# Kernel tuning notes

Measured on AMD Instinct MI355X. Metric: run time of the kernel, lower is better.

## Reference

```python
import jax, jax.numpy as jnp
import numpy as np

N_HEAD = 16
N_STATE = 1024
D_HEAD = N_STATE // N_HEAD
B, T = 4, 2048


def setup_inputs() -> dict:
    key = jax.random.key(0)
    ks = jax.random.split(key, 9)
    x = jax.random.normal(ks[0], (B, T, N_STATE), dtype=jnp.float32)
    # causal additive mask, (T, T)
    neg = jnp.float32(-1e9)
    mask = jnp.where(jnp.tril(jnp.ones((T, T), dtype=bool)), 0.0, neg).astype(jnp.float32)
    s = 0.02  # keep activations in a sane range (module uses torch.randn init)
    Wq = jax.random.normal(ks[1], (N_STATE, N_STATE), dtype=jnp.float32) * s
    bq = jax.random.normal(ks[2], (N_STATE,), dtype=jnp.float32) * s
    Wk = jax.random.normal(ks[3], (N_STATE, N_STATE), dtype=jnp.float32) * s
    Wv = jax.random.normal(ks[4], (N_STATE, N_STATE), dtype=jnp.float32) * s
    bv = jax.random.normal(ks[5], (N_STATE,), dtype=jnp.float32) * s
    Wo = jax.random.normal(ks[6], (N_STATE, N_STATE), dtype=jnp.float32) * s
    bo = jax.random.normal(ks[7], (N_STATE,), dtype=jnp.float32) * s
    return {"x": x, "mask": mask, "Wq": Wq, "bq": bq, "Wk": Wk,
            "Wv": Wv, "bv": bv, "Wo": Wo, "bo": bo}


def reference(x, mask, Wq, bq, Wk, Wv, bv, Wo, bo):
    n, t, _ = x.shape
    scale = D_HEAD ** -0.25
    # projections: Linear stores weight as (out, in), applies x @ W.T
    q = x @ Wq.T + bq
    k = x @ Wk.T          # key has no bias
    v = x @ Wv.T + bv
    # (N, H, T, d)
    q = q.reshape(n, t, N_HEAD, D_HEAD).transpose(0, 2, 1, 3) * scale
    k = k.reshape(n, t, N_HEAD, D_HEAD).transpose(0, 2, 1, 3) * scale
    v = v.reshape(n, t, N_HEAD, D_HEAD).transpose(0, 2, 1, 3)
    qk = jnp.einsum('bhqd,bhkd->bhqk', q, k)
    qk = qk + mask[:t, :t]
    attn = jax.nn.softmax(qk, axis=-1)
    qkv = jnp.einsum('bhqk,bhkd->bhqd', attn, v)
    qkv = qkv.transpose(0, 2, 1, 3).reshape(n, t, N_STATE)
    return qkv @ Wo.T + bo
```

## Files before the change

kernel.cpp:

```cpp
#include <hip/hip_runtime.h>
#include <stdint.h>

#define DEVI __device__ __forceinline__

typedef float        f32x4   __attribute__((ext_vector_type(4)));
typedef float        f32x16  __attribute__((ext_vector_type(16)));
typedef __bf16       bf16x8  __attribute__((ext_vector_type(8)));
typedef unsigned short u16x8 __attribute__((ext_vector_type(8)));
typedef uint32_t     u32x2   __attribute__((ext_vector_type(2)));
typedef uint32_t     u32x4   __attribute__((ext_vector_type(4)));

static constexpr int TSEQ   = 2048;
static constexpr int NSTATE = 1024;
static constexpr int NHEAD  = 16;
static constexpr int DHEAD  = 64;
static constexpr int BATCH  = 4;
static constexpr int MROWS  = BATCH * TSEQ;
static constexpr float QSCALE = 0.125f * 1.44269504088896340736f;
static constexpr float DEFER_THR = 8.0f * 1.44269504088896340736f;

DEVI unsigned short f2bf(float f) {
  union { float f; uint32_t u; } v; v.f = f;
  return (unsigned short)((v.u + 0x7fffu + ((v.u >> 16) & 1u)) >> 16);
}

DEVI uint32_t cvt_pk_bf16(float lo, float hi) {
  uint32_t r;
  asm("v_cvt_pk_bf16_f32 %0, %1, %2" : "=v"(r) : "v"(lo), "v"(hi));
  return r;
}

DEVI f32x4 mfma16(u16x8 a, u16x8 b, f32x4 c) {
  return __builtin_amdgcn_mfma_f32_16x16x32_bf16(
      __builtin_bit_cast(bf16x8, a), __builtin_bit_cast(bf16x8, b), c, 0, 0, 0);
}
DEVI f32x16 mfma32(u16x8 a, u16x8 b, f32x16 c) {
  return __builtin_amdgcn_mfma_f32_32x32x16_bf16(
      __builtin_bit_cast(bf16x8, a), __builtin_bit_cast(bf16x8, b), c, 0, 0, 0);
}

DEVI void gload_lds16(const void* g, void* l) {
  __builtin_amdgcn_global_load_lds(
      (const __attribute__((address_space(1))) void*)g,
      (__attribute__((address_space(3))) void*)l, 16, 0, 0);
}

__global__ void cvt_kernel(const float* __restrict__ in,
                           unsigned short* __restrict__ out, int n4) {
  int i = blockIdx.x * blockDim.x + threadIdx.x;
  const int stride = gridDim.x * blockDim.x;
  for (; i < n4; i += stride) {
    const float4 f = ((const float4*)in)[i];
    ushort4 o;
    o.x = f2bf(f.x); o.y = f2bf(f.y); o.z = f2bf(f.z); o.w = f2bf(f.w);
    ((ushort4*)out)[i] = o;
  }
}

__global__ void cvt4_kernel(const float* __restrict__ w0, const float* __restrict__ w1,
                            const float* __restrict__ w2, const float* __restrict__ w3,
                            unsigned short* __restrict__ o0, unsigned short* __restrict__ o1,
                            unsigned short* __restrict__ o2, unsigned short* __restrict__ o3) {
  const int per = NSTATE * NSTATE / 4;
  int i = blockIdx.x * blockDim.x + threadIdx.x;
  const int stride = gridDim.x * blockDim.x;
  for (; i < 4 * per; i += stride) {
    const int wi = i / per, j = i - wi * per;
    const float* src = (wi == 0) ? w0 : (wi == 1) ? w1 : (wi == 2) ? w2 : w3;
    unsigned short* dst = (wi == 0) ? o0 : (wi == 1) ? o1 : (wi == 2) ? o2 : o3;
    const float4 f = ((const float4*)src)[j];
    ushort4 o;
    o.x = f2bf(f.x); o.y = f2bf(f.y); o.z = f2bf(f.z); o.w = f2bf(f.w);
    ((ushort4*)dst)[j] = o;
  }
}

__global__ __launch_bounds__(256)
void gemm_qkv(const unsigned short* __restrict__ A,
              const unsigned short* __restrict__ Wqkv,
              const float* __restrict__ bq, const float* __restrict__ bv,
              unsigned short* __restrict__ Oqkv)
{
  __shared__ __align__(16) unsigned short As[128 * 32];
  __shared__ __align__(16) unsigned short Bs[128 * 32];
  const int t  = threadIdx.x;
  const int l  = t & 63, w = t >> 6;
  const int fr = l & 15, fq = l >> 4;
  const int wi = blockIdx.x >> 3;
  const int n0 = (blockIdx.x & 7) * 128;
  const int m0 = blockIdx.y * 128;
  const int wm = (w & 1) * 64, wn = (w >> 1) * 64;
  const unsigned short* Bw = Wqkv + (size_t)wi * (1u << 20);
  unsigned short* Cq = Oqkv + (size_t)wi * (8u << 20);

  f32x4 acc[4][4] = {};

  const int sr = t >> 2;
  const int sc = (t & 3) * 8;
  const unsigned short* ag = A  + (size_t)(m0 + sr) * NSTATE + sc;
  const unsigned short* bg = Bw + (size_t)(n0 + sr) * NSTATE + sc;
  unsigned short* lA0 = As + t * 8;
  unsigned short* lA1 = As + 2048 + t * 8;
  unsigned short* lB0 = Bs + t * 8;
  unsigned short* lB1 = Bs + 2048 + t * 8;

  for (int kt = 0; kt < NSTATE / 32; ++kt) {
    const int ko = kt * 32;
    gload_lds16(ag + ko,               lA0);
    gload_lds16(ag + 64 * NSTATE + ko, lA1);
    gload_lds16(bg + ko,               lB0);
    gload_lds16(bg + 64 * NSTATE + ko, lB1);
    __syncthreads();

    u16x8 a[4], b[4];
    #pragma unroll
    for (int i = 0; i < 4; ++i)
      a[i] = *(const u16x8*)(As + (wm + i * 16 + fr) * 32 + fq * 8);
    #pragma unroll
    for (int j = 0; j < 4; ++j)
      b[j] = *(const u16x8*)(Bs + (wn + j * 16 + fr) * 32 + fq * 8);
    #pragma unroll
    for (int i = 0; i < 4; ++i)
      #pragma unroll
      for (int j = 0; j < 4; ++j)
        acc[i][j] = mfma16(a[i], b[j], acc[i][j]);
    __syncthreads();
  }

  const int h = (n0 + wn) >> 6;
  #pragma unroll
  for (int j = 0; j < 4; ++j) {
    const int d = j * 16 + fr;
    const float bj = (wi == 1) ? 0.0f
                   : ((wi == 0) ? bq[n0 + wn + d] : bv[n0 + wn + d]);
    #pragma unroll
    for (int i = 0; i < 4; ++i) {
      #pragma unroll
      for (int r = 0; r < 4; ++r) {
        const int row = m0 + wm + i * 16 + fq * 4 + r;
        const int bb = row >> 11, tt = row & (TSEQ - 1);
        float v = acc[i][j][r] + bj;
        if (wi == 0) v *= QSCALE;
        Cq[(((size_t)(bb * NHEAD + h)) * TSEQ + tt) * DHEAD + d] = f2bf(v);
      }
    }
  }
}

__global__ __launch_bounds__(256)
void gemm_out(const unsigned short* __restrict__ A,
              const unsigned short* __restrict__ Bw,
              const float* __restrict__ bias,
              float* __restrict__ Co)
{
  __shared__ __align__(16) unsigned short As[128 * 32];
  __shared__ __align__(16) unsigned short Bs[128 * 32];
  const int t  = threadIdx.x;
  const int l  = t & 63, w = t >> 6;
  const int fr = l & 15, fq = l >> 4;
  const int m0 = blockIdx.y * 128, n0 = blockIdx.x * 128;
  const int wm = (w & 1) * 64, wn = (w >> 1) * 64;

  f32x4 acc[4][4] = {};

  const int sr = t >> 2;
  const int sc = (t & 3) * 8;
  const unsigned short* ag = A  + (size_t)(m0 + sr) * NSTATE + sc;
  const unsigned short* bg = Bw + (size_t)(n0 + sr) * NSTATE + sc;
  unsigned short* lA0 = As + t * 8;
  unsigned short* lA1 = As + 2048 + t * 8;
  unsigned short* lB0 = Bs + t * 8;
  unsigned short* lB1 = Bs + 2048 + t * 8;

  for (int kt = 0; kt < NSTATE / 32; ++kt) {
    const int ko = kt * 32;
    gload_lds16(ag + ko,               lA0);
    gload_lds16(ag + 64 * NSTATE + ko, lA1);
    gload_lds16(bg + ko,               lB0);
    gload_lds16(bg + 64 * NSTATE + ko, lB1);
    __syncthreads();

    u16x8 a[4], b[4];
    #pragma unroll
    for (int i = 0; i < 4; ++i)
      a[i] = *(const u16x8*)(As + (wm + i * 16 + fr) * 32 + fq * 8);
    #pragma unroll
    for (int j = 0; j < 4; ++j)
      b[j] = *(const u16x8*)(Bs + (wn + j * 16 + fr) * 32 + fq * 8);
    #pragma unroll
    for (int i = 0; i < 4; ++i)
      #pragma unroll
      for (int j = 0; j < 4; ++j)
        acc[i][j] = mfma16(a[i], b[j], acc[i][j]);
    __syncthreads();
  }

  #pragma unroll
  for (int j = 0; j < 4; ++j) {
    const int col = n0 + wn + j * 16 + fr;
    const float bj = bias[col];
    #pragma unroll
    for (int i = 0; i < 4; ++i) {
      const int row0 = m0 + wm + i * 16 + fq * 4;
      #pragma unroll
      for (int r = 0; r < 4; ++r)
        Co[(size_t)(row0 + r) * NSTATE + col] = acc[i][j][r] + bj;
    }
  }
}

__global__ __launch_bounds__(256)
void flash_attn(const unsigned short* __restrict__ Qg,
                const unsigned short* __restrict__ Kg,
                const unsigned short* __restrict__ Vg,
                unsigned short* __restrict__ O)
{
  const int bh = blockIdx.x;
  const int qb = 15 - (int)blockIdx.y;
  const int b  = bh >> 4, h = bh & 15;
  const int t  = threadIdx.x, lane = t & 63, w = t >> 6;
  const int lq = lane & 31, hi = lane >> 5;
  const size_t hoff = (size_t)bh * TSEQ * DHEAD;
  const unsigned short* Qp = Qg + hoff;
  const unsigned short* Kp = Kg + hoff;
  const unsigned short* Vp = Vg + hoff;

  __shared__ __align__(16) unsigned short Kb[2][64 * 64];
  __shared__ __align__(16) unsigned short Vb[2][64 * 64];

  const int qw   = qb * 128 + w * 32;
  const int qrow = qw + lq;

  u16x8 qf[4];
  #pragma unroll
  for (int c = 0; c < 4; ++c)
    qf[c] = *(const u16x8*)(Qp + (size_t)qrow * DHEAD + c * 16 + hi * 8);

  f32x16 oacc[2] = {};
  float m_r = -1e30f, l_r = 0.0f;

  const int skr = t >> 2, skg = t & 3;
  const int svk2 = (t & 31) * 2;
  const int svd  = (t >> 5) * 8;

  const int nt = (qb + 1) * 2;

  {
    const u16x8 kr0 = *(const u16x8*)(Kp + (size_t)skr * DHEAD + skg * 16);
    const u16x8 kr1 = *(const u16x8*)(Kp + (size_t)skr * DHEAD + skg * 16 + 8);
    const u16x8 va  = *(const u16x8*)(Vp + (size_t)svk2 * DHEAD + svd);
    const u16x8 vb  = *(const u16x8*)(Vp + (size_t)(svk2 + 1) * DHEAD + svd);
    *(u16x8*)(&Kb[0][skr * 64 + (((skg * 2)     ^ (skr & 7)) << 3)]) = kr0;
    *(u16x8*)(&Kb[0][skr * 64 + (((skg * 2 + 1) ^ (skr & 7)) << 3)]) = kr1;
    #pragma unroll
    for (int i = 0; i < 8; ++i)
      *(uint32_t*)(&Vb[0][(svd + i) * 64 + (svk2 ^ (i << 3))]) =
          (uint32_t)va[i] | ((uint32_t)vb[i] << 16);
  }
  __syncthreads();

  for (int kt = 0; kt < nt; ++kt) {
    const int k0 = kt * 64, cur = kt & 1;
    const bool pre = (kt + 1 < nt);
    u16x8 krn0, krn1, van, vbn;
    if (pre) {
      const int k0n = k0 + 64;
      krn0 = *(const u16x8*)(Kp + (size_t)(k0n + skr) * DHEAD + skg * 16);
      krn1 = *(const u16x8*)(Kp + (size_t)(k0n + skr) * DHEAD + skg * 16 + 8);
      van  = *(const u16x8*)(Vp + (size_t)(k0n + svk2) * DHEAD + svd);
      vbn  = *(const u16x8*)(Vp + (size_t)(k0n + svk2 + 1) * DHEAD + svd);
    }

    if (k0 < qw + 32) {
      f32x16 s[2];
      __builtin_amdgcn_s_setprio(1);
      #pragma unroll
      for (int t32 = 0; t32 < 2; ++t32) {
        if (k0 + t32 * 32 < qw + 32) {
          f32x16 z = {};
          #pragma unroll
          for (int c = 0; c < 4; ++c) {
            const u16x8 kf = *(const u16x8*)(
                &Kb[cur][(t32 * 32 + lq) * 64 + (((2 * c + hi) ^ (lane & 7)) << 3)]);
            z = mfma32(kf, qf[c], z);
          }
          s[t32] = z;
        } else {
          #pragma unroll
          for (int r = 0; r < 16; ++r) s[t32][r] = -1e30f;
        }
      }
      __builtin_amdgcn_s_setprio(0);
      if (k0 + 63 > qw) {
        #pragma unroll
        for (int t32 = 0; t32 < 2; ++t32)
          #pragma unroll
          for (int r = 0; r < 16; ++r) {
            const int kk = k0 + t32 * 32 + (r & 3) + 8 * (r >> 2) + 4 * hi;
            if (kk > qrow) s[t32][r] = -1e30f;
          }
      }

      float mx = fmaxf(s[0][14], s[0][15]);
      #pragma unroll
      for (int r = 0; r < 14; r += 2) mx = fmaxf(fmaxf(mx, s[0][r]), s[0][r + 1]);
      #pragma unroll
      for (int r = 0; r < 16; r += 2) mx = fmaxf(fmaxf(mx, s[1][r]), s[1][r + 1]);
      mx = fmaxf(mx, __shfl_xor(mx, 32));

      if (__any(mx > m_r + DEFER_THR)) {
        const float mnew = fmaxf(m_r, mx);
        const float corr = exp2f(m_r - mnew);
        #pragma unroll
        for (int ds = 0; ds < 2; ++ds)
          #pragma unroll
          for (int r = 0; r < 16; ++r) oacc[ds][r] *= corr;
        l_r *= corr;
        m_r = mnew;
      }

      float ps = 0.0f;
      uint32_t pk[2][8];
      #pragma unroll
      for (int t32 = 0; t32 < 2; ++t32)
        #pragma unroll
        for (int m2 = 0; m2 < 8; ++m2) {
          const float pa = exp2f(s[t32][2 * m2]     - m_r);
          const float pb = exp2f(s[t32][2 * m2 + 1] - m_r);
          ps += pa + pb;
          pk[t32][m2] = cvt_pk_bf16(pa, pb);
        }
      ps += __shfl_xor(ps, 32);
      l_r += ps;

      uint32_t pf[2][2][4];
      #pragma unroll
      for (int t32 = 0; t32 < 2; ++t32)
        #pragma unroll
        for (int hf = 0; hf < 2; ++hf) {
          const u32x2 r02 = __builtin_amdgcn_permlane32_swap(
              pk[t32][hf * 4 + 0], pk[t32][hf * 4 + 2], false, false);
          const u32x2 r13 = __builtin_amdgcn_permlane32_swap(
              pk[t32][hf * 4 + 1], pk[t32][hf * 4 + 3], false, false);
          pf[t32][hf][0] = r02.x; pf[t32][hf][2] = r02.y;
          pf[t32][hf][1] = r13.x; pf[t32][hf][3] = r13.y;
        }

      __builtin_amdgcn_s_setprio(1);
      #pragma unroll
      for (int c = 0; c < 4; ++c) {
        if (k0 + 16 * c < qw + 32) {
          const u32x4 pw = {pf[c >> 1][c & 1][0], pf[c >> 1][c & 1][1],
                            pf[c >> 1][c & 1][2], pf[c >> 1][c & 1][3]};
          const u16x8 pv = __builtin_bit_cast(u16x8, pw);
          #pragma unroll
          for (int ds = 0; ds < 2; ++ds) {
            const u16x8 vf = *(const u16x8*)(
                &Vb[cur][(ds * 32 + lq) * 64 + (((2 * c + hi) ^ (lq & 7)) << 3)]);
            oacc[ds] = mfma32(vf, pv, oacc[ds]);
          }
        }
      }
      __builtin_amdgcn_s_setprio(0);
    }

    if (pre) {
      *(u16x8*)(&Kb[cur ^ 1][skr * 64 + (((skg * 2)     ^ (skr & 7)) << 3)]) = krn0;
      *(u16x8*)(&Kb[cur ^ 1][skr * 64 + (((skg * 2 + 1) ^ (skr & 7)) << 3)]) = krn1;
      #pragma unroll
      for (int i = 0; i < 8; ++i)
        *(uint32_t*)(&Vb[cur ^ 1][(svd + i) * 64 + (svk2 ^ (i << 3))]) =
            (uint32_t)van[i] | ((uint32_t)vbn[i] << 16);
    }
    __syncthreads();
  }

  const float inv = 1.0f / l_r;
  const size_t base = ((size_t)(b * TSEQ + qrow)) * NSTATE + h * DHEAD;
  #pragma unroll
  for (int ds = 0; ds < 2; ++ds)
    #pragma unroll
    for (int m2 = 0; m2 < 8; ++m2) {
      const int d = ds * 32 + 2 * (m2 & 1) + 8 * (m2 >> 1) + 4 * hi;
      *(uint32_t*)(O + base + d) =
          cvt_pk_bf16(oacc[ds][2 * m2] * inv, oacc[ds][2 * m2 + 1] * inv);
    }
}

extern "C" void kernel_launch(void* const* d_in, const int* in_sizes, int n_in,
                              void* d_out, int out_size, void* d_ws, size_t ws_size,
                              hipStream_t stream)
{
  (void)in_sizes; (void)n_in; (void)out_size; (void)ws_size;
  const float* x  = (const float*)d_in[0];
  const float* Wq = (const float*)d_in[2];
  const float* bq = (const float*)d_in[3];
  const float* Wk = (const float*)d_in[4];
  const float* Wv = (const float*)d_in[5];
  const float* bv = (const float*)d_in[6];
  const float* Wo = (const float*)d_in[7];
  const float* bo = (const float*)d_in[8];

  char* ws = (char*)d_ws;
  unsigned short* xb  = (unsigned short*)(ws);
  unsigned short* wqb = (unsigned short*)(ws + (16u << 20));
  unsigned short* wkb = wqb + (1u << 20);
  unsigned short* wvb = wkb + (1u << 20);
  unsigned short* wob = wvb + (1u << 20);
  unsigned short* qb_ = (unsigned short*)(ws + (24u << 20));
  unsigned short* kb_ = (unsigned short*)(ws + (40u << 20));
  unsigned short* vb_ = (unsigned short*)(ws + (56u << 20));

  cvt_kernel<<<2048, 256, 0, stream>>>(x,  xb,  MROWS * NSTATE / 4);
  cvt4_kernel<<<2048, 256, 0, stream>>>(Wq, Wk, Wv, Wo, wqb, wkb, wvb, wob);

  gemm_qkv<<<dim3(24, MROWS / 128), 256, 0, stream>>>(xb, wqb, bq, bv, qb_);

  flash_attn<<<dim3(BATCH * NHEAD, 16), 256, 0, stream>>>(qb_, kb_, vb_, xb);

  gemm_out<<<dim3(NSTATE / 128, MROWS / 128), 256, 0, stream>>>(xb, wob, bo, (float*)d_out);
}
```

Before: 199.3 us.

## Double-buffer GEMM LDS tiles, MFMA row sums and reordered causal tiles in attention

Both projection GEMMs now use two LDS buffers. The next K-slice is prefetched with global-to-LDS loads while MFMAs run on the current one, removing one barrier per iteration. The attention kernel computes the softmax row sum with an extra MFMA against a ones matrix instead of VALU adds plus a cross-lane shuffle. It also packs V into LDS with byte-permute instructions and interleaves query-block order across the grid to balance causal work. The cost is doubled LDS use in the GEMMs, which may lower occupancy, and extra MFMA issue in attention.

Measured after the change: 219.8 us. 1.1x slower.

```diff
diff --git a/kernel.cpp b/kernel.cpp
--- a/kernel.cpp
+++ b/kernel.cpp
@@ -81,8 +81,8 @@
               const float* __restrict__ bq, const float* __restrict__ bv,
               unsigned short* __restrict__ Oqkv)
 {
-  __shared__ __align__(16) unsigned short As[128 * 32];
-  __shared__ __align__(16) unsigned short Bs[128 * 32];
+  __shared__ __align__(16) unsigned short As[2][128 * 32];
+  __shared__ __align__(16) unsigned short Bs[2][128 * 32];
   const int t  = threadIdx.x;
   const int l  = t & 63, w = t >> 6;
   const int fr = l & 15, fq = l >> 4;
@@ -99,26 +99,30 @@
   const int sc = (t & 3) * 8;
   const unsigned short* ag = A  + (size_t)(m0 + sr) * NSTATE + sc;
   const unsigned short* bg = Bw + (size_t)(n0 + sr) * NSTATE + sc;
-  unsigned short* lA0 = As + t * 8;
-  unsigned short* lA1 = As + 2048 + t * 8;
-  unsigned short* lB0 = Bs + t * 8;
-  unsigned short* lB1 = Bs + 2048 + t * 8;
-
+
+  #define STAGE_G(buf, ko)                                              \
+    do {                                                                \
+      gload_lds16(ag + (ko),               &As[buf][t * 8]);            \
+      gload_lds16(ag + 64 * NSTATE + (ko), &As[buf][2048 + t * 8]);     \
+      gload_lds16(bg + (ko),               &Bs[buf][t * 8]);            \
+      gload_lds16(bg + 64 * NSTATE + (ko), &Bs[buf][2048 + t * 8]);     \
+    } while (0)
+
+  STAGE_G(0, 0);
+  __syncthreads();
+
+  #pragma unroll 2
   for (int kt = 0; kt < NSTATE / 32; ++kt) {
-    const int ko = kt * 32;
-    gload_lds16(ag + ko,               lA0);
-    gload_lds16(ag + 64 * NSTATE + ko, lA1);
-    gload_lds16(bg + ko,               lB0);
-    gload_lds16(bg + 64 * NSTATE + ko, lB1);
-    __syncthreads();
+    const int cur = kt & 1;
+    if (kt + 1 < NSTATE / 32) STAGE_G(cur ^ 1, (kt + 1) * 32);
 
     u16x8 a[4], b[4];
     #pragma unroll
     for (int i = 0; i < 4; ++i)
-      a[i] = *(const u16x8*)(As + (wm + i * 16 + fr) * 32 + fq * 8);
+      a[i] = *(const u16x8*)(&As[cur][(wm + i * 16 + fr) * 32 + fq * 8]);
     #pragma unroll
     for (int j = 0; j < 4; ++j)
-      b[j] = *(const u16x8*)(Bs + (wn + j * 16 + fr) * 32 + fq * 8);
+      b[j] = *(const u16x8*)(&Bs[cur][(wn + j * 16 + fr) * 32 + fq * 8]);
     #pragma unroll
     for (int i = 0; i < 4; ++i)
       #pragma unroll
@@ -153,8 +157,8 @@
               const float* __restrict__ bias,
               float* __restrict__ Co)
 {
-  __shared__ __align__(16) unsigned short As[128 * 32];
-  __shared__ __align__(16) unsigned short Bs[128 * 32];
+  __shared__ __align__(16) unsigned short As[2][128 * 32];
+  __shared__ __align__(16) unsigned short Bs[2][128 * 32];
   const int t  = threadIdx.x;
   const int l  = t & 63, w = t >> 6;
   const int fr = l & 15, fq = l >> 4;
@@ -167,26 +171,22 @@
   const int sc = (t & 3) * 8;
   const unsigned short* ag = A  + (size_t)(m0 + sr) * NSTATE + sc;
   const unsigned short* bg = Bw + (size_t)(n0 + sr) * NSTATE + sc;
-  unsigned short* lA0 = As + t * 8;
-  unsigned short* lA1 = As + 2048 + t * 8;
-  unsigned short* lB0 = Bs + t * 8;
-  unsigned short* lB1 = Bs + 2048 + t * 8;
-
+
+  STAGE_G(0, 0);
+  __syncthreads();
+
+  #pragma unroll 2
   for (int kt = 0; kt < NSTATE / 32; ++kt) {
-    const int ko = kt * 32;
-    gload_lds16(ag + ko,               lA0);
-    gload_lds16(ag + 64 * NSTATE + ko, lA1);
-    gload_lds16(bg + ko,               lB0);
-    gload_lds16(bg + 64 * NSTATE + ko, lB1);
-    __syncthreads();
+    const int cur = kt & 1;
+    if (kt + 1 < NSTATE / 32) STAGE_G(cur ^ 1, (kt + 1) * 32);
 
     u16x8 a[4], b[4];
     #pragma unroll
     for (int i = 0; i < 4; ++i)
-      a[i] = *(const u16x8*)(As + (wm + i * 16 + fr) * 32 + fq * 8);
+      a[i] = *(const u16x8*)(&As[cur][(wm + i * 16 + fr) * 32 + fq * 8]);
     #pragma unroll
     for (int j = 0; j < 4; ++j)
-      b[j] = *(const u16x8*)(Bs + (wn + j * 16 + fr) * 32 + fq * 8);
+      b[j] = *(const u16x8*)(&Bs[cur][(wn + j * 16 + fr) * 32 + fq * 8]);
     #pragma unroll
     for (int i = 0; i < 4; ++i)
       #pragma unroll
@@ -216,7 +216,8 @@
                 unsigned short* __restrict__ O)
 {
   const int bh = blockIdx.x;
-  const int qb = 15 - (int)blockIdx.y;
+  const int yy = blockIdx.y, ai = yy & 3, ii = yy >> 2;
+  const int qb = (ii == 0) ? 15 - ai : (ii == 1) ? ai : (ii == 2) ? 8 + ai : 7 - ai;
   const int b  = bh >> 4, h = bh & 15;
   const int t  = threadIdx.x, lane = t & 63, w = t >> 6;
   const int lq = lane & 31, hi = lane >> 5;
@@ -236,14 +237,31 @@
   for (int c = 0; c < 4; ++c)
     qf[c] = *(const u16x8*)(Qp + (size_t)qrow * DHEAD + c * 16 + hi * 8);
 
+  const u16x8 ones8 = {0x3F80, 0x3F80, 0x3F80, 0x3F80,
+                       0x3F80, 0x3F80, 0x3F80, 0x3F80};
+
   f32x16 oacc[2] = {};
-  float m_r = -1e30f, l_r = 0.0f;
+  f32x16 lacc = {};
+  float m_r = -1e30f;
 
   const int skr = t >> 2, skg = t & 3;
   const int svk2 = (t & 31) * 2;
   const int svd  = (t >> 5) * 8;
 
   const int nt = (qb + 1) * 2;
+
+  #define STAGE_V(buf, va, vb)                                              \
+    do {                                                                    \
+      const u32x4 vau = __builtin_bit_cast(u32x4, va);                      \
+      const u32x4 vbu = __builtin_bit_cast(u32x4, vb);                      \
+      _Pragma("unroll")                                                     \
+      for (int j = 0; j < 4; ++j) {                                         \
+        const uint32_t pe = __builtin_amdgcn_perm(vbu[j], vau[j], 0x05040100); \
+        const uint32_t po = __builtin_amdgcn_perm(vbu[j], vau[j], 0x07060302); \
+        *(uint32_t*)(&Vb[buf][(svd + 2 * j) * 64 + (svk2 ^ ((2 * j) << 3))]) = pe; \
+        *(uint32_t*)(&Vb[buf][(svd + 2 * j + 1) * 64 + (svk2 ^ ((2 * j + 1) << 3))]) = po; \
+      }                                                                     \
+    } while (0)
 
   {
     const u16x8 kr0 = *(const u16x8*)(Kp + (size_t)skr * DHEAD + skg * 16);
@@ -252,10 +270,7 @@
     const u16x8 vb  = *(const u16x8*)(Vp + (size_t)(svk2 + 1) * DHEAD + svd);
     *(u16x8*)(&Kb[0][skr * 64 + (((skg * 2)     ^ (skr & 7)) << 3)]) = kr0;
     *(u16x8*)(&Kb[0][skr * 64 + (((skg * 2 + 1) ^ (skr & 7)) << 3)]) = kr1;
-    #pragma unroll
-    for (int i = 0; i < 8; ++i)
-      *(uint32_t*)(&Vb[0][(svd + i) * 64 + (svk2 ^ (i << 3))]) =
-          (uint32_t)va[i] | ((uint32_t)vb[i] << 16);
+    STAGE_V(0, va, vb);
   }
   __syncthreads();
 
@@ -315,11 +330,10 @@
         for (int ds = 0; ds < 2; ++ds)
           #pragma unroll
           for (int r = 0; r < 16; ++r) oacc[ds][r] *= corr;
-        l_r *= corr;
+        lacc[0] *= corr;
         m_r = mnew;
       }
 
-      float ps = 0.0f;
       uint32_t pk[2][8];
       #pragma unroll
       for (int t32 = 0; t32 < 2; ++t32)
@@ -327,11 +341,8 @@
         for (int m2 = 0; m2 < 8; ++m2) {
           const float pa = exp2f(s[t32][2 * m2]     - m_r);
           const float pb = exp2f(s[t32][2 * m2 + 1] - m_r);
-          ps += pa + pb;
           pk[t32][m2] = cvt_pk_bf16(pa, pb);
         }
-      ps += __shfl_xor(ps, 32);
-      l_r += ps;
 
       uint32_t pf[2][2][4];
       #pragma unroll
@@ -359,6 +370,7 @@
                 &Vb[cur][(ds * 32 + lq) * 64 + (((2 * c + hi) ^ (lq & 7)) << 3)]);
             oacc[ds] = mfma32(vf, pv, oacc[ds]);
           }
+          lacc = mfma32(ones8, pv, lacc);
         }
       }
       __builtin_amdgcn_s_setprio(0);
@@ -367,15 +379,12 @@
     if (pre) {
       *(u16x8*)(&Kb[cur ^ 1][skr * 64 + (((skg * 2)     ^ (skr & 7)) << 3)]) = krn0;
       *(u16x8*)(&Kb[cur ^ 1][skr * 64 + (((skg * 2 + 1) ^ (skr & 7)) << 3)]) = krn1;
-      #pragma unroll
-      for (int i = 0; i < 8; ++i)
-        *(uint32_t*)(&Vb[cur ^ 1][(svd + i) * 64 + (svk2 ^ (i << 3))]) =
-            (uint32_t)van[i] | ((uint32_t)vbn[i] << 16);
+      STAGE_V(cur ^ 1, van, vbn);
     }
     __syncthreads();
   }
 
-  const float inv = 1.0f / l_r;
+  const float inv = 1.0f / lacc[0];
   const size_t base = ((size_t)(b * TSEQ + qrow)) * NSTATE + h * DHEAD;
   #pragma unroll
   for (int ds = 0; ds < 2; ++ds)
```
